# Kernel tuning notes

Measured on AMD Instinct MI355X. Metric: run time of the kernel, lower is better.

The kernel has to match this reference:

```python
import jax, jax.numpy as jnp
import numpy as np

RATIOS = [0.9, 0.7, 0.5, 0.3]
EPS = 1e-5


def _layernorm(x, g, b):
    m = jnp.mean(x, axis=-1, keepdims=True)
    v = jnp.mean(jnp.square(x - m), axis=-1, keepdims=True)
    return (x - m) * jax.lax.rsqrt(v + EPS) * g + b


def _stage(x, g, b, W, bias):
    return _layernorm(x, g, b) @ W + bias


def _prune(x, W1, b1, W2, b2, ratio):
    B, N, C = x.shape
    stats = jnp.mean(x, axis=1)                       # (B, C)
    scores = jax.nn.relu(stats @ W1 + b1) @ W2 + b2    # (B, C)
    k = max(1, int(C * ratio))
    _, idx = jax.lax.top_k(jax.lax.stop_gradient(scores), k)  # (B, k)
    hard = jnp.zeros((B, C), scores.dtype).at[jnp.arange(B)[:, None], idx].set(1.0)
    soft = jax.nn.sigmoid(scores)
    # straight-through: forward value == hard, gradient flows through soft
    mask = hard + soft - jax.lax.stop_gradient(soft)
    return x * mask[:, None, :]


def setup_inputs() -> dict:
    key = jax.random.key(0)
    dims = [(96, 96), (96, 192), (192, 384), (384, 768)]
    inp = {}
    ks = jax.random.split(key, 64)
    ki = iter(ks)
    inp["x"] = jax.random.normal(next(ki), (32, 3136, 96), dtype=jnp.float32)
    for i, (din, dout) in enumerate(dims, 1):
        inp[f"s{i}_g"] = jnp.ones((din,), jnp.float32)
        inp[f"s{i}_b"] = jnp.zeros((din,), jnp.float32)
        inp[f"s{i}_W"] = jax.random.normal(next(ki), (din, dout), jnp.float32) * 0.02
        inp[f"s{i}_bias"] = jnp.zeros((dout,), jnp.float32)
        d = dout
        inp[f"p{i}_W1"] = jax.random.normal(next(ki), (d, d // 4), jnp.float32) * 0.02
        inp[f"p{i}_b1"] = jnp.zeros((d // 4,), jnp.float32)
        inp[f"p{i}_W2"] = jax.random.normal(next(ki), (d // 4, d), jnp.float32) * 0.02
        inp[f"p{i}_b2"] = jnp.zeros((d,), jnp.float32)
    inp["H"] = 56
    inp["W"] = 56
    return inp


def reference(x,
              s1_g, s1_b, s1_W, s1_bias, p1_W1, p1_b1, p1_W2, p1_b2,
              s2_g, s2_b, s2_W, s2_bias, p2_W1, p2_b1, p2_W2, p2_b2,
              s3_g, s3_b, s3_W, s3_bias, p3_W1, p3_b1, p3_W2, p3_b2,
              s4_g, s4_b, s4_W, s4_bias, p4_W1, p4_b1, p4_W2, p4_b2,
              H, W):
    x = _stage(x, s1_g, s1_b, s1_W, s1_bias)
    x = _prune(x, p1_W1, p1_b1, p1_W2, p1_b2, RATIOS[0])
    x = _stage(x, s2_g, s2_b, s2_W, s2_bias)
    x = _prune(x, p2_W1, p2_b1, p2_W2, p2_b2, RATIOS[1])
    x = _stage(x, s3_g, s3_b, s3_W, s3_bias)
    x = _prune(x, p3_W1, p3_b1, p3_W2, p3_b2, RATIOS[2])
    x = _stage(x, s4_g, s4_b, s4_W, s4_bias)
    x = _prune(x, p4_W1, p4_b1, p4_W2, p4_b2, RATIOS[3])
    return x
```

## Files before the change

### kernel.cpp

```cpp
#include <hip/hip_runtime.h>
#include <hip/hip_bf16.h>
#include <stdint.h>

#define NTOK 3136
#define MTOT 100352
#define RPW  14
#define WPB  224

typedef __attribute__((ext_vector_type(8))) short bf16x8;
typedef __attribute__((ext_vector_type(4))) float f32x4;
typedef __attribute__((ext_vector_type(2))) float f32x2;

static __device__ __forceinline__ ushort f2bf(float x) {
  union { float f; uint32_t u; } c; c.f = x;
  uint32_t r = (c.u + 0x7FFFu + ((c.u >> 16) & 1u)) >> 16;
  return (ushort)r;
}
static __device__ __forceinline__ float bf2f(ushort h) {
  union { uint32_t u; float f; } c; c.u = ((uint32_t)h) << 16;
  return c.f;
}

template<int DIN, bool WLO>
__global__ __launch_bounds__(256)
void ln_colsum_k(const float* __restrict__ in, const float* __restrict__ gma,
                 const float* __restrict__ bta, ushort* __restrict__ oh,
                 ushort* __restrict__ ol, float* __restrict__ part)
{
  constexpr int P2 = DIN / 2;
  constexpr int T2 = (P2 + 63) / 64;
  const int wid  = (blockIdx.x * 256 + threadIdx.x) >> 6;
  const int lane = threadIdx.x & 63;
  const int b = wid / WPB;
  const int w = wid - b * WPB;

  f32x2 gv[T2], bv[T2], acc[T2];
#pragma unroll
  for (int t = 0; t < T2; ++t) {
    int c2 = lane + 64 * t;
    if (c2 < P2) {
      gv[t] = *(const f32x2*)(gma + 2 * c2);
      bv[t] = *(const f32x2*)(bta + 2 * c2);
    } else { gv[t] = {0.f, 0.f}; bv[t] = {0.f, 0.f}; }
    acc[t] = {0.f, 0.f};
  }

  const size_t rbase = ((size_t)b * NTOK + (size_t)w * RPW) * DIN;
  const float* ip = in + rbase;
  ushort* oph = oh + rbase;
  ushort* opl = ol + rbase;

  for (int j = 0; j < RPW; ++j) {
    f32x2 v[T2];
    float s = 0.f, sq = 0.f;
#pragma unroll
    for (int t = 0; t < T2; ++t) {
      int c2 = lane + 64 * t;
      f32x2 xv = {0.f, 0.f};
      if (c2 < P2) xv = *(const f32x2*)(ip + (size_t)j * DIN + 2 * c2);
      v[t] = xv;
      s  += xv[0] + xv[1];
      sq += xv[0] * xv[0] + xv[1] * xv[1];
    }
#pragma unroll
    for (int off = 1; off < 64; off <<= 1) {
      s  += __shfl_xor(s, off);
      sq += __shfl_xor(sq, off);
    }
    float m   = s / (float)DIN;
    float var = sq / (float)DIN - m * m;
    float r   = 1.f / sqrtf(var + 1e-5f);
#pragma unroll
    for (int t = 0; t < T2; ++t) {
      int c2 = lane + 64 * t;
      if (c2 < P2) {
        float xn0 = (v[t][0] - m) * r * gv[t][0] + bv[t][0];
        float xn1 = (v[t][1] - m) * r * gv[t][1] + bv[t][1];
        ushort h0 = f2bf(xn0), h1 = f2bf(xn1);
        ((uint32_t*)(oph + (size_t)j * DIN))[c2] =
            (uint32_t)h0 | ((uint32_t)h1 << 16);
        if (WLO) {
          ushort l0 = f2bf(xn0 - bf2f(h0)), l1 = f2bf(xn1 - bf2f(h1));
          ((uint32_t*)(opl + (size_t)j * DIN))[c2] =
              (uint32_t)l0 | ((uint32_t)l1 << 16);
        }
        acc[t][0] += xn0;
        acc[t][1] += xn1;
      }
    }
  }
#pragma unroll
  for (int t = 0; t < T2; ++t) {
    int c2 = lane + 64 * t;
    if (c2 < P2) {
      int c = 2 * c2;
      part[((size_t)b * DIN + c) * WPB + w]     = acc[t][0];
      part[((size_t)b * DIN + c + 1) * WPB + w] = acc[t][1];
    }
  }
}

template<int DIN, int DOUT, int SLOTS, bool CMP, int CMPN>
__global__ __launch_bounds__(1024)
void scores_k(const float* __restrict__ part,
              const float* __restrict__ Wt, const float* __restrict__ bias,
              const float* __restrict__ W1, const float* __restrict__ b1,
              const float* __restrict__ W2, const float* __restrict__ b2,
              float* __restrict__ mask, int k,
              int* __restrict__ list_g, float* __restrict__ biasc)
{
  constexpr int DH  = DOUT / 4;
  constexpr int DH4 = DH / 4;
  constexpr int NSLC = (1024 / DH4 < 64) ? 1024 / DH4 : 64;
  constexpr int RPSC = (DOUT + NSLC - 1) / NSLC;
  constexpr int C4  = DOUT / 4;
  constexpr int NSLD = (1024 / C4 < 64) ? 1024 / C4 : 64;
  constexpr int RPSD = (DH + NSLD - 1) / NSLD;

  __shared__ float xm[DIN];
  __shared__ float st[DOUT];
  __shared__ float h[DH];
  __shared__ float sc[DOUT];
  __shared__ float red[4096];
  __shared__ int lsh[256];

  const int b = blockIdx.x, tid = threadIdx.x;

  if constexpr (SLOTS == 25) {
    if (tid < DIN) {
      const float* p = part + ((size_t)b * DIN + tid) * 25;
      float s = 0.f;
#pragma unroll
      for (int i = 0; i < 25; ++i) s += p[i];
      xm[tid] = s * (1.f / (float)NTOK);
    }
  } else {
    const int cg = tid >> 2, wq = tid & 3;
    if (cg < DIN) {
      const float* p = part + ((size_t)b * DIN + cg) * WPB + wq * 56;
      f32x4 a = {0.f, 0.f, 0.f, 0.f};
#pragma unroll
      for (int u = 0; u < 14; ++u) {
        f32x4 t0 = *(const f32x4*)(p + u * 4);
        a[0] += t0[0]; a[1] += t0[1]; a[2] += t0[2]; a[3] += t0[3];
      }
      red[wq * DIN + cg] = (a[0] + a[1]) + (a[2] + a[3]);
    }
    __syncthreads();
    if (tid < DIN)
      xm[tid] = ((red[0 * DIN + tid] + red[1 * DIN + tid]) +
                 (red[2 * DIN + tid] + red[3 * DIN + tid])) * (1.f / (float)NTOK);
  }
  __syncthreads();

  {
    constexpr int RPS = DIN / 4;
    const int j4 = tid % C4, sl = tid / C4;
    if (sl < 4) {
      const float* wp = Wt + (size_t)(sl * RPS) * DOUT + j4 * 4;
      f32x4 acc = {0.f, 0.f, 0.f, 0.f};
#pragma unroll
      for (int r = 0; r < RPS; ++r) {
        f32x4 wv = *(const f32x4*)(wp + (size_t)r * DOUT);
        float xv = xm[sl * RPS + r];
        acc[0] = fmaf(xv, wv[0], acc[0]);
        acc[1] = fmaf(xv, wv[1], acc[1]);
        acc[2] = fmaf(xv, wv[2], acc[2]);
        acc[3] = fmaf(xv, wv[3], acc[3]);
      }
      *(f32x4*)&red[sl * DOUT + j4 * 4] = acc;
    }
  }
  __syncthreads();
  if (tid < DOUT)
    st[tid] = ((red[0 * DOUT + tid] + red[1 * DOUT + tid]) +
               (red[2 * DOUT + tid] + red[3 * DOUT + tid])) + bias[tid];
  __syncthreads();

  {
    const int j4 = tid % DH4, sl = tid / DH4;
    if (sl < NSLC) {
      f32x4 acc = {0.f, 0.f, 0.f, 0.f};
#pragma unroll
      for (int rr = 0; rr < RPSC; ++rr) {
        int r = sl * RPSC + rr;
        if (r < DOUT) {
          f32x4 wv = *(const f32x4*)(W1 + (size_t)r * DH + j4 * 4);
          float sv = st[r];
          acc[0] = fmaf(sv, wv[0], acc[0]);
          acc[1] = fmaf(sv, wv[1], acc[1]);
          acc[2] = fmaf(sv, wv[2], acc[2]);
          acc[3] = fmaf(sv, wv[3], acc[3]);
        }
      }
      *(f32x4*)&red[(size_t)sl * DH + j4 * 4] = acc;
    }
  }
  __syncthreads();
  if (tid < DH) {
    float a = 0.f;
#pragma unroll 4
    for (int sl = 0; sl < NSLC; ++sl) a += red[(size_t)sl * DH + tid];
    h[tid] = fmaxf(b1[tid] + a, 0.f);
  }
  __syncthreads();

  {
    const int c4 = tid % C4, sl = tid / C4;
    if (sl < NSLD) {
      f32x4 acc = {0.f, 0.f, 0.f, 0.f};
#pragma unroll
      for (int rr = 0; rr < RPSD; ++rr) {
        int r = sl * RPSD + rr;
        if (r < DH) {
          f32x4 wv = *(const f32x4*)(W2 + (size_t)r * DOUT + c4 * 4);
          float hv = h[r];
          acc[0] = fmaf(hv, wv[0], acc[0]);
          acc[1] = fmaf(hv, wv[1], acc[1]);
          acc[2] = fmaf(hv, wv[2], acc[2]);
          acc[3] = fmaf(hv, wv[3], acc[3]);
        }
      }
      *(f32x4*)&red[(size_t)sl * DOUT + c4 * 4] = acc;
    }
  }
  __syncthreads();
  for (int c = tid; c < DOUT; c += 1024) {
    float a = 0.f;
#pragma unroll 4
    for (int sl = 0; sl < NSLD; ++sl) a += red[(size_t)sl * DOUT + c];
    sc[c] = b2[c] + a;
  }
  __syncthreads();

  for (int c = tid; c < DOUT; c += 1024) {
    float v = sc[c];
    int rank = 0;
#pragma unroll 8
    for (int j = 0; j < DOUT; ++j) {
      float u = sc[j];
      rank += (u > v) || (u == v && j < c);
    }
    mask[(size_t)b * DOUT + c] = (rank < k) ? 1.f : 0.f;
    if (CMP && rank < k) lsh[rank] = c;
  }
  if constexpr (CMP) {
    if (tid >= k && tid < CMPN) lsh[tid] = -1;
    __syncthreads();
    if (tid < CMPN) {
      int c = lsh[tid];
      list_g[b * 256 + tid] = c;
      biasc[b * 256 + tid] = (c >= 0) ? bias[c] : 0.f;
    }
  }
}

__global__ __launch_bounds__(256)
void convW_all_k(const float* __restrict__ W0, const float* __restrict__ W1,
                 const float* __restrict__ W2, const float* __restrict__ W3,
                 ushort* __restrict__ hi, ushort* __restrict__ lo)
{
  const int Kd[4]   = { 96, 96, 192, 384 };
  const int Nd[4]   = { 96, 192, 384, 768 };
  const int off[5]  = { 0, 12288, 36864, 110592, 405504 };
  const float* Wp[4] = { W0, W1, W2, W3 };

  int idx = blockIdx.x * 256 + threadIdx.x;
  if (idx >= 405504) return;
  int s = (idx >= off[1]) + (idx >= off[2]) + (idx >= off[3]);
  int local = idx - off[s];
  int K = Kd[s], N = Nd[s];
  int n = local / K, kk = local - n * K;
  float v = (n < N) ? Wp[s][(size_t)kk * N + n] : 0.f;
  ushort h = f2bf(v);
  hi[idx] = h;
  lo[idx] = f2bf(v - bf2f(h));
}

#define ASYNC16(GP, LP) __builtin_amdgcn_global_load_lds( \
    (const __attribute__((address_space(1))) void*)(GP),  \
    (__attribute__((address_space(3))) void*)(LP), 16, 0, 0)

template<int K, int BNL, int N, int NWN, bool WLO>
__global__ __launch_bounds__(128 * NWN)
void gemm_ln_k(const ushort* __restrict__ ahi, const ushort* __restrict__ alo,
               const ushort* __restrict__ bhi, const ushort* __restrict__ blo,
               const float* __restrict__ bias, const float* __restrict__ msk,
               const float* __restrict__ gnext, const float* __restrict__ bnext,
               ushort* __restrict__ oh, ushort* __restrict__ ol,
               float* __restrict__ part)
{
  constexpr int T   = 128 * NWN;
  constexpr int R   = T / 4;
  constexpr int AI  = 128 / R;
  constexpr int BI  = BNL / R;
  constexpr int KS  = K / 32;
  constexpr int WN  = N / NWN;
  constexpr int NFR = WN / 16;
  __shared__ __align__(16) ushort ldsAh[128 * 32];
  __shared__ __align__(16) ushort ldsAl[128 * 32];
  __shared__ __align__(16) ushort ldsBh[BNL * 32];
  __shared__ __align__(16) ushort ldsBl[BNL * 32];

  const int tid  = threadIdx.x;
  const int lane = tid & 63;
  const int wid  = tid >> 6;
  const int wm = wid & 1, wn = wid >> 1;

  const int q8  = gridDim.x >> 3;
  const int bid = blockIdx.x;
  const int mt  = (bid & 7) * q8 + (bid >> 3);
  const size_t row0 = (size_t)mt * 128;

  f32x4 acc[4][NFR];
#pragma unroll
  for (int i = 0; i < 4; ++i)
#pragma unroll
    for (int j = 0; j < NFR; ++j) acc[i][j] = { 0.f, 0.f, 0.f, 0.f };

  const int c_row  = tid >> 2;
  const int c_phys = tid & 3;

#define STG(KK)                                                                \
  {                                                                            \
    const int k0_ = (KK) * 32;                                                 \
    _Pragma("unroll")                                                          \
    for (int r_ = 0; r_ < AI; ++r_) {                                          \
      int row_  = c_row + r_ * R;                                              \
      int slot_ = c_phys ^ ((row_ >> 1) & 3);                                  \
      ASYNC16(ahi + (row0 + row_) * (size_t)K + (k0_ + slot_ * 8),             \
              &ldsAh[(row_ * 4 + c_phys) * 8]);                                \
      ASYNC16(alo + (row0 + row_) * (size_t)K + (k0_ + slot_ * 8),             \
              &ldsAl[(row_ * 4 + c_phys) * 8]);                                \
    }                                                                          \
    _Pragma("unroll")                                                          \
    for (int r_ = 0; r_ < BI; ++r_) {                                          \
      int row_  = c_row + r_ * R;                                              \
      int slot_ = c_phys ^ ((row_ >> 1) & 3);                                  \
      ASYNC16(bhi + (size_t)row_ * K + (k0_ + slot_ * 8),                      \
              &ldsBh[(row_ * 4 + c_phys) * 8]);                                \
      ASYNC16(blo + (size_t)row_ * K + (k0_ + slot_ * 8),                      \
              &ldsBl[(row_ * 4 + c_phys) * 8]);                                \
    }                                                                          \
  }

#pragma unroll
  for (int t = 0; t < KS; ++t) {
    STG(t);
    asm volatile("s_waitcnt vmcnt(0)" ::: "memory");
    __builtin_amdgcn_s_barrier();
    const int slot = lane >> 4;
    const int r16  = lane & 15;
    bf16x8 ah[4], al[4], bh[NFR], bl[NFR];
#pragma unroll
    for (int mi = 0; mi < 4; ++mi) {
      int r = wm * 64 + mi * 16 + r16;
      int off = (r * 4 + (slot ^ ((r >> 1) & 3))) * 8;
      ah[mi] = *(const bf16x8*)&ldsAh[off];
      al[mi] = *(const bf16x8*)&ldsAl[off];
    }
#pragma unroll
    for (int ni = 0; ni < NFR; ++ni) {
      int r = wn * WN + ni * 16 + r16;
      int off = (r * 4 + (slot ^ ((r >> 1) & 3))) * 8;
      bh[ni] = *(const bf16x8*)&ldsBh[off];
      bl[ni] = *(const bf16x8*)&ldsBl[off];
    }
#pragma unroll
    for (int mi = 0; mi < 4; ++mi)
#pragma unroll
      for (int ni = 0; ni < NFR; ++ni)
        acc[mi][ni] = __builtin_amdgcn_mfma_f32_16x16x32_bf16(ah[mi], bh[ni],
                                                              acc[mi][ni], 0, 0, 0);
#pragma unroll
    for (int mi = 0; mi < 4; ++mi)
#pragma unroll
      for (int ni = 0; ni < NFR; ++ni)
        acc[mi][ni] = __builtin_amdgcn_mfma_f32_16x16x32_bf16(ah[mi], bl[ni],
                                                              acc[mi][ni], 0, 0, 0);
#pragma unroll
    for (int mi = 0; mi < 4; ++mi)
#pragma unroll
      for (int ni = 0; ni < NFR; ++ni)
        acc[mi][ni] = __builtin_amdgcn_mfma_f32_16x16x32_bf16(al[mi], bh[ni],
                                                              acc[mi][ni], 0, 0, 0);
    if (t + 1 < KS) __builtin_amdgcn_s_barrier();
  }
#undef STG

  __syncthreads();

  float* rowred = (float*)&ldsAh[0];
  float* colred = (float*)&ldsAl[0];
  ushort* xsh = (ushort*)&ldsBh[0];
  ushort* xsl = (ushort*)&ldsBl[0];

  const int l15 = lane & 15, l4 = lane >> 4;
  const int b0i = (int)(row0 / NTOK);
  const size_t rowB = (size_t)(b0i + 1) * NTOK;
  const bool strad = rowB < row0 + 128;

  float biasv[NFR], mk0a[NFR], mk1a[NFR], gvn[NFR], bvn[NFR];
#pragma unroll
  for (int ni = 0; ni < NFR; ++ni) {
    int n = wn * WN + ni * 16 + l15;
    biasv[ni] = bias[n];
    mk0a[ni] = msk[(size_t)b0i * N + n];
    mk1a[ni] = strad ? msk[(size_t)(b0i + 1) * N + n] : mk0a[ni];
    gvn[ni] = gnext[n];
    bvn[ni] = bnext[n];
  }

  float rs[16], rq[16];
#pragma unroll
  for (int i = 0; i < 16; ++i) { rs[i] = 0.f; rq[i] = 0.f; }
#pragma unroll
  for (int mi = 0; mi < 4; ++mi)
#pragma unroll
    for (int q = 0; q < 4; ++q) {
      size_t row = row0 + wm * 64 + mi * 16 + l4 * 4 + q;
      bool loB = row < rowB;
#pragma unroll
      for (int ni = 0; ni < NFR; ++ni) {
        float v = (acc[mi][ni][q] + biasv[ni]) * (loB ? mk0a[ni] : mk1a[ni]);
        acc[mi][ni][q] = v;
        rs[mi * 4 + q] += v;
        rq[mi * 4 + q] += v * v;
      }
    }
#pragma unroll
  for (int off = 1; off < 16; off <<= 1)
#pragma unroll
    for (int i = 0; i < 16; ++i) {
      rs[i] += __shfl_xor(rs[i], off);
      rq[i] += __shfl_xor(rq[i], off);
    }
  if (l15 == 0) {
#pragma unroll
    for (int mi = 0; mi < 4; ++mi)
#pragma unroll
      for (int q = 0; q < 4; ++q) {
        int r = wm * 64 + mi * 16 + l4 * 4 + q;
        rowred[(wn * 128 + r) * 2 + 0] = rs[mi * 4 + q];
        rowred[(wn * 128 + r) * 2 + 1] = rq[mi * 4 + q];
      }
  }
  __syncthreads();

  float mean[16], rstd[16];
#pragma unroll
  for (int mi = 0; mi < 4; ++mi)
#pragma unroll
    for (int q = 0; q < 4; ++q) {
      int r = wm * 64 + mi * 16 + l4 * 4 + q;
      float S = 0.f, Q = 0.f;
#pragma unroll
      for (int w = 0; w < NWN; ++w) {
        S += rowred[(w * 128 + r) * 2 + 0];
        Q += rowred[(w * 128 + r) * 2 + 1];
      }
      float mn  = S / (float)N;
      float var = Q / (float)N - mn * mn;
      mean[mi * 4 + q] = mn;
      rstd[mi * 4 + q] = 1.f / sqrtf(var + 1e-5f);
    }

  float cs0[NFR], cs1[NFR];
#pragma unroll
  for (int ni = 0; ni < NFR; ++ni) { cs0[ni] = 0.f; cs1[ni] = 0.f; }
#pragma unroll
  for (int mi = 0; mi < 4; ++mi) {
    __syncthreads();
#pragma unroll
    for (int q = 0; q < 4; ++q) {
      const int rl = l4 * 4 + q;
      const size_t row = row0 + wm * 64 + mi * 16 + rl;
      const bool loB = row < rowB;
      const float mn = mean[mi * 4 + q], rv = rstd[mi * 4 + q];
#pragma unroll
      for (int ni = 0; ni < NFR; ++ni) {
        const int n = wn * WN + ni * 16 + l15;
        float xn = (acc[mi][ni][q] - mn) * rv * gvn[ni] + bvn[ni];
        ushort hh = f2bf(xn);
        xsh[(wm * 16 + rl) * N + n] = hh;
        if constexpr (WLO) xsl[(wm * 16 + rl) * N + n] = f2bf(xn - bf2f(hh));
        if (loB) cs0[ni] += xn; else cs1[ni] += xn;
      }
    }
    __syncthreads();
    constexpr int U4R = N / 8;
    for (int idx = tid; idx < 32 * U4R; idx += T) {
      const int grp = idx / U4R, c = idx - grp * U4R;
      const size_t row = row0 + (grp >> 4) * 64 + mi * 16 + (grp & 15);
      *(uint4*)(oh + row * (size_t)N + c * 8) =
          *(const uint4*)(xsh + grp * N + c * 8);
      if constexpr (WLO)
        *(uint4*)(ol + row * (size_t)N + c * 8) =
            *(const uint4*)(xsl + grp * N + c * 8);
    }
  }

#pragma unroll
  for (int ni = 0; ni < NFR; ++ni) {
    cs0[ni] += __shfl_xor(cs0[ni], 16);
    cs0[ni] += __shfl_xor(cs0[ni], 32);
    cs1[ni] += __shfl_xor(cs1[ni], 16);
    cs1[ni] += __shfl_xor(cs1[ni], 32);
  }
  __syncthreads();
  if (l4 == 0) {
#pragma unroll
    for (int ni = 0; ni < NFR; ++ni) {
      int n = wn * WN + ni * 16 + l15;
      colred[(0 * 2 + wm) * N + n] = cs0[ni];
      colred[(1 * 2 + wm) * N + n] = cs1[ni];
    }
  }
  __syncthreads();
  if (wm == 0 && l4 == 0) {
    const int mt_lo = (b0i * NTOK) >> 7;
    const int slot0 = mt - mt_lo;
#pragma unroll
    for (int ni = 0; ni < NFR; ++ni) {
      int n = wn * WN + ni * 16 + l15;
      float t0 = colred[0 * N + n] + colred[1 * N + n];
      part[((size_t)b0i * N + n) * 25 + slot0] = t0;
      if (strad) {
        float t1 = colred[2 * N + n] + colred[3 * N + n];
        part[((size_t)(b0i + 1) * N + n) * 25 + 0] = t1;
      }
    }
  }
}

template<int K, int NC, int N>
__global__ __launch_bounds__(256)
void gemm_lnc_k(const ushort* __restrict__ ahi, const ushort* __restrict__ alo,
                const ushort* __restrict__ whi, const ushort* __restrict__ wlo,
                const int* __restrict__ list, const float* __restrict__ biasc,
                const float* __restrict__ gnext, const float* __restrict__ bnext,
                ushort* __restrict__ oh, float* __restrict__ part)
{
  constexpr int KS  = K / 32;
  constexpr int WN  = NC / 2;
  constexpr int NFR = WN / 16;
  __shared__ __align__(16) ushort ldsAh[2][128 * 32];
  __shared__ __align__(16) ushort ldsAl[2][128 * 32];
  __shared__ __align__(16) ushort ldsBh[2][NC * 32];
  __shared__ __align__(16) ushort ldsBl[2][NC * 32];

  const int tid  = threadIdx.x;
  const int lane = tid & 63;
  const int wid  = tid >> 6;
  const int wm = wid & 1, wn = wid >> 1;

  const int q8  = gridDim.x >> 3;
  const int bid = blockIdx.x;
  const int wg  = (bid & 7) * q8 + (bid >> 3);
  const int b   = wg / 25;
  const int mt  = wg - b * 25;
  const size_t row0 = (size_t)b * NTOK + (size_t)mt * 128;
  const size_t rowEnd = (size_t)(b + 1) * NTOK;
  const int rows_valid = (mt == 24) ? 64 : 128;

  const int c_row  = tid >> 2;
  const int c_phys = tid & 3;

  int bsrc[3];
#pragma unroll
  for (int r_ = 0; r_ < 3; ++r_) {
    int s = list[b * 256 + c_row + r_ * 64];
    bsrc[r_] = (s < 0) ? 0 : s;
  }

  f32x4 acc[4][NFR];
#pragma unroll
  for (int i = 0; i < 4; ++i)
#pragma unroll
    for (int j = 0; j < NFR; ++j) acc[i][j] = { 0.f, 0.f, 0.f, 0.f };

#define STGL(BUF, KK)                                                          \
  {                                                                            \
    const int k0_ = (KK) * 32;                                                 \
    _Pragma("unroll")                                                          \
    for (int r_ = 0; r_ < 2; ++r_) {                                           \
      int row_  = c_row + r_ * 64;                                             \
      int slot_ = c_phys ^ ((row_ >> 1) & 3);                                  \
      size_t ar_ = row0 + row_;                                                \
      if (ar_ >= rowEnd) ar_ = rowEnd - 1;                                     \
      ASYNC16(ahi + ar_ * (size_t)K + (k0_ + slot_ * 8),                       \
              &ldsAh[BUF][(row_ * 4 + c_phys) * 8]);                           \
      ASYNC16(alo + ar_ * (size_t)K + (k0_ + slot_ * 8),                       \
              &ldsAl[BUF][(row_ * 4 + c_phys) * 8]);                           \
    }                                                                          \
    _Pragma("unroll")                                                          \
    for (int r_ = 0; r_ < 3; ++r_) {                                           \
      int row_  = c_row + r_ * 64;                                             \
      int slot_ = c_phys ^ ((row_ >> 1) & 3);                                  \
      ASYNC16(whi + (size_t)bsrc[r_] * K + (k0_ + slot_ * 8),                  \
              &ldsBh[BUF][(row_ * 4 + c_phys) * 8]);                           \
      ASYNC16(wlo + (size_t)bsrc[r_] * K + (k0_ + slot_ * 8),                  \
              &ldsBl[BUF][(row_ * 4 + c_phys) * 8]);                           \
    }                                                                          \
  }

  STGL(0, 0);
  asm volatile("s_waitcnt vmcnt(0)" ::: "memory");
  __builtin_amdgcn_s_barrier();
#pragma unroll
  for (int t = 0; t < KS; ++t) {
    if (t + 1 < KS) STGL((t + 1) & 1, t + 1);
    const int buf = t & 1;
    const int slot = lane >> 4;
    const int r16  = lane & 15;
    bf16x8 ah[4], al[4], bh[NFR], bl[NFR];
#pragma unroll
    for (int mi = 0; mi < 4; ++mi) {
      int r = wm * 64 + mi * 16 + r16;
      int off = (r * 4 + (slot ^ ((r >> 1) & 3))) * 8;
      ah[mi] = *(const bf16x8*)&ldsAh[buf][off];
      al[mi] = *(const bf16x8*)&ldsAl[buf][off];
    }
#pragma unroll
    for (int ni = 0; ni < NFR; ++ni) {
      int r = wn * WN + ni * 16 + r16;
      int off = (r * 4 + (slot ^ ((r >> 1) & 3))) * 8;
      bh[ni] = *(const bf16x8*)&ldsBh[buf][off];
      bl[ni] = *(const bf16x8*)&ldsBl[buf][off];
    }
#pragma unroll
    for (int mi = 0; mi < 4; ++mi)
#pragma unroll
      for (int ni = 0; ni < NFR; ++ni)
        acc[mi][ni] = __builtin_amdgcn_mfma_f32_16x16x32_bf16(ah[mi], bh[ni],
                                                              acc[mi][ni], 0, 0, 0);
#pragma unroll
    for (int mi = 0; mi < 4; ++mi)
#pragma unroll
      for (int ni = 0; ni < NFR; ++ni)
        acc[mi][ni] = __builtin_amdgcn_mfma_f32_16x16x32_bf16(ah[mi], bl[ni],
                                                              acc[mi][ni], 0, 0, 0);
#pragma unroll
    for (int mi = 0; mi < 4; ++mi)
#pragma unroll
      for (int ni = 0; ni < NFR; ++ni)
        acc[mi][ni] = __builtin_amdgcn_mfma_f32_16x16x32_bf16(al[mi], bh[ni],
                                                              acc[mi][ni], 0, 0, 0);
    if (t + 1 < KS) {
      asm volatile("s_waitcnt vmcnt(0)" ::: "memory");
      __builtin_amdgcn_s_barrier();
    }
  }
#undef STGL

  __syncthreads();

  float* rr      = (float*)&ldsAh[0][0];
  float* rowredp = rr;
  float* rowmnrv = rr + 512;
  float* rowrv   = rr + 640;
  float* sbuf    = (float*)&ldsBh[0][0];

  const int l15 = lane & 15, l4 = lane >> 4;

  int   nj[NFR];
  float biasv[NFR];
#pragma unroll
  for (int ni = 0; ni < NFR; ++ni) {
    int j = wn * WN + ni * 16 + l15;
    nj[ni]    = list[b * 256 + j];
    biasv[ni] = biasc[b * 256 + j];
  }

  float rs[16], rq[16];
#pragma unroll
  for (int i = 0; i < 16; ++i) { rs[i] = 0.f; rq[i] = 0.f; }
#pragma unroll
  for (int mi = 0; mi < 4; ++mi)
#pragma unroll
    for (int q = 0; q < 4; ++q) {
#pragma unroll
      for (int ni = 0; ni < NFR; ++ni) {
        float v = acc[mi][ni][q] + biasv[ni];
        acc[mi][ni][q] = v;
        rs[mi * 4 + q] += v;
        rq[mi * 4 + q] += v * v;
      }
    }
#pragma unroll
  for (int off = 1; off < 16; off <<= 1)
#pragma unroll
    for (int i = 0; i < 16; ++i) {
      rs[i] += __shfl_xor(rs[i], off);
      rq[i] += __shfl_xor(rq[i], off);
    }
  if (l15 == 0) {
#pragma unroll
    for (int mi = 0; mi < 4; ++mi)
#pragma unroll
      for (int q = 0; q < 4; ++q) {
        int r = wm * 64 + mi * 16 + l4 * 4 + q;
        rowredp[(wn * 128 + r) * 2 + 0] = rs[mi * 4 + q];
        rowredp[(wn * 128 + r) * 2 + 1] = rq[mi * 4 + q];
      }
  }
  __syncthreads();
  if (tid < 128) {
    float S = rowredp[(0 * 128 + tid) * 2 + 0] + rowredp[(1 * 128 + tid) * 2 + 0];
    float Q = rowredp[(0 * 128 + tid) * 2 + 1] + rowredp[(1 * 128 + tid) * 2 + 1];
    float mn = S / (float)N;
    float rv = 1.f / sqrtf(Q / (float)N - mn * mn + 1e-5f);
    rowmnrv[tid] = mn * rv;
    rowrv[tid]   = rv;
  }
  __syncthreads();

  float colS = 0.f, colS2 = 0.f;

#pragma unroll
  for (int h = 0; h < 8; ++h) {
    if (h * 16 >= rows_valid) break;
    __syncthreads();
    for (int idx = tid; idx < 16 * N / 4; idx += 256)
      ((f32x4*)sbuf)[idx] = f32x4{0.f, 0.f, 0.f, 0.f};
    __syncthreads();
    if ((h >> 2) == wm) {
      const int mi = h & 3;
#pragma unroll
      for (int q = 0; q < 4; ++q) {
        const int rl = l4 * 4 + q;
        const float rv = rowrv[h * 16 + rl];
#pragma unroll
        for (int ni = 0; ni < NFR; ++ni)
          sbuf[rl * N + nj[ni]] = acc[mi][ni][q] * rv;
      }
    }
    __syncthreads();
    {
      float a = 0.f;
#pragma unroll
      for (int rl = 0; rl < 16; ++rl) a += sbuf[rl * N + tid];
      colS += a;
      if (tid < N - 256) {
        float a2 = 0.f;
        const int c2 = 256 + tid;
#pragma unroll
        for (int rl = 0; rl < 16; ++rl) a2 += sbuf[rl * N + c2];
        colS2 += a2;
      }
    }
    for (int idx = tid; idx < 16 * (N / 8); idx += 256) {
      const int rl = idx / (N / 8), cg = idx - rl * (N / 8);
      const float mnrv = rowmnrv[h * 16 + rl];
      const float* sp = sbuf + rl * N + cg * 8;
      f32x4 s0 = *(const f32x4*)(sp);
      f32x4 s1 = *(const f32x4*)(sp + 4);
      f32x4 g0 = *(const f32x4*)(gnext + cg * 8);
      f32x4 g1 = *(const f32x4*)(gnext + cg * 8 + 4);
      f32x4 e0 = *(const f32x4*)(bnext + cg * 8);
      f32x4 e1 = *(const f32x4*)(bnext + cg * 8 + 4);
      uint32_t w[4];
#pragma unroll
      for (int j = 0; j < 2; ++j) {
        ushort ha = f2bf(g0[2*j]   * (s0[2*j]   - mnrv) + e0[2*j]);
        ushort hb = f2bf(g0[2*j+1] * (s0[2*j+1] - mnrv) + e0[2*j+1]);
        w[j] = (uint32_t)ha | ((uint32_t)hb << 16);
      }
#pragma unroll
      for (int j = 0; j < 2; ++j) {
        ushort ha = f2bf(g1[2*j]   * (s1[2*j]   - mnrv) + e1[2*j]);
        ushort hb = f2bf(g1[2*j+1] * (s1[2*j+1] - mnrv) + e1[2*j+1]);
        w[2 + j] = (uint32_t)ha | ((uint32_t)hb << 16);
      }
      *(uint4*)(oh + (row0 + h * 16 + rl) * (size_t)N + cg * 8) =
          make_uint4(w[0], w[1], w[2], w[3]);
    }
  }

  float msum = 0.f;
  for (int r = 0; r < rows_valid; ++r) msum += rowmnrv[r];
  {
    const int c = tid;
    part[((size_t)b * N + c) * 25 + mt] =
        gnext[c] * (colS - msum) + (float)rows_valid * bnext[c];
    if (tid < N - 256) {
      const int c2 = 256 + tid;
      part[((size_t)b * N + c2) * 25 + mt] =
          gnext[c2] * (colS2 - msum) + (float)rows_valid * bnext[c2];
    }
  }
}

template<int K>
__global__ __launch_bounds__(512)
void gemm_c4_k(const ushort* __restrict__ A, const ushort* __restrict__ whi,
               const int* __restrict__ list, const float* __restrict__ biasc,
               float* __restrict__ C)
{
  constexpr int NT = K / 32;
  __shared__ __align__(16) ushort ldsA[3][128 * 32];
  __shared__ __align__(16) ushort ldsB[3][256 * 32];

  const int tid  = threadIdx.x;
  const int lane = tid & 63;
  const int wid  = tid >> 6;
  const int wm = wid & 1, wn = wid >> 1;

  const int q8  = gridDim.x >> 3;
  const int bid = blockIdx.x;
  const int wg  = (bid & 7) * q8 + (bid >> 3);
  const int b   = wg / 25;
  const int mt  = wg - b * 25;
  const size_t row0 = (size_t)b * NTOK + (size_t)mt * 128;
  const int rows_valid = (mt == 24) ? 64 : 128;

  const int c_row  = tid >> 2;
  const int c_phys = tid & 3;

  size_t arow = row0 + c_row;
  const size_t rowEnd = (size_t)(b + 1) * NTOK;
  if (arow >= rowEnd) arow = rowEnd - 1;
  const ushort* apr = A + arow * (size_t)K;

  int bsrc[2];
#pragma unroll
  for (int r_ = 0; r_ < 2; ++r_) {
    int s = list[b * 256 + c_row + r_ * 128];
    bsrc[r_] = (s < 0) ? 0 : s;
  }

  f32x4 acc[4][4];
#pragma unroll
  for (int i = 0; i < 4; ++i)
#pragma unroll
    for (int j = 0; j < 4; ++j) acc[i][j] = { 0.f, 0.f, 0.f, 0.f };

#define STAGEC(BUF, TT)                                                        \
  {                                                                            \
    const int k0_ = (TT) * 32;                                                 \
    {                                                                          \
      int slot_ = c_phys ^ ((c_row >> 1) & 3);                                 \
      ASYNC16(apr + (k0_ + slot_ * 8),                                         \
              &ldsA[BUF][(c_row * 4 + c_phys) * 8]);                           \
    }                                                                          \
    _Pragma("unroll")                                                          \
    for (int r_ = 0; r_ < 2; ++r_) {                                           \
      int row_  = c_row + r_ * 128;                                            \
      int slot_ = c_phys ^ ((row_ >> 1) & 3);                                  \
      ASYNC16(whi + (size_t)bsrc[r_] * K + (k0_ + slot_ * 8),                  \
              &ldsB[BUF][(row_ * 4 + c_phys) * 8]);                            \
    }                                                                          \
  }

  STAGEC(0, 0);
  STAGEC(1, 1);
#pragma unroll
  for (int t = 0; t < NT; ++t) {
    if (t == NT - 1) { asm volatile("s_waitcnt vmcnt(0)" ::: "memory"); }
    else             { asm volatile("s_waitcnt vmcnt(3)" ::: "memory"); }
    __builtin_amdgcn_s_barrier();
    if (t + 2 < NT) STAGEC((t + 2) % 3, t + 2);
    const int buf = t % 3;
    const int slot = lane >> 4;
    const int r16  = lane & 15;
    bf16x8 af[4], bfr[4];
#pragma unroll
    for (int mi = 0; mi < 4; ++mi) {
      int r = wm * 64 + mi * 16 + r16;
      af[mi] = *(const bf16x8*)&ldsA[buf][(r * 4 + (slot ^ ((r >> 1) & 3))) * 8];
    }
#pragma unroll
    for (int ni = 0; ni < 4; ++ni) {
      int r = wn * 64 + ni * 16 + r16;
      bfr[ni] = *(const bf16x8*)&ldsB[buf][(r * 4 + (slot ^ ((r >> 1) & 3))) * 8];
    }
#pragma unroll
    for (int mi = 0; mi < 4; ++mi)
#pragma unroll
      for (int ni = 0; ni < 4; ++ni)
        acc[mi][ni] = __builtin_amdgcn_mfma_f32_16x16x32_bf16(af[mi], bfr[ni],
                                                              acc[mi][ni], 0, 0, 0);
  }
#undef STAGEC

  float* cst = (float*)&ldsB[0][0];

  const int l15 = lane & 15, l4 = lane >> 4;
  int   nj[4];
  float biasv[4];
#pragma unroll
  for (int ni = 0; ni < 4; ++ni) {
    int j = wn * 64 + ni * 16 + l15;
    nj[ni]    = list[b * 256 + j];
    biasv[ni] = biasc[b * 256 + j];
  }

#pragma unroll
  for (int hh = 0; hh < 8; ++hh) {
    const int hrows = rows_valid - hh * 16;
    if (hrows <= 0) break;
    __syncthreads();
    for (int idx = tid; idx < 16 * 192; idx += 512)
      ((f32x4*)cst)[idx] = f32x4{0.f, 0.f, 0.f, 0.f};
    __syncthreads();
    if ((hh >> 2) == wm) {
      const int mi = hh & 3;
#pragma unroll
      for (int q = 0; q < 4; ++q) {
        const int rl = l4 * 4 + q;
#pragma unroll
        for (int ni = 0; ni < 4; ++ni)
          if (nj[ni] >= 0)
            cst[rl * 768 + nj[ni]] = acc[mi][ni][q] + biasv[ni];
      }
    }
    __syncthreads();
    const int nst = (hrows >= 16 ? 16 : hrows) * 192;
    for (int idx = tid; idx < nst; idx += 512) {
      const int grp = idx / 192, c = idx - grp * 192;
      const size_t row = row0 + hh * 16 + grp;
      *(f32x4*)(C + row * 768 + c * 4) = ((const f32x4*)cst)[grp * 192 + c];
    }
  }
}

extern "C" void kernel_launch(void* const* d_in, const int* in_sizes, int n_in,
                              void* d_out, int out_size, void* d_ws, size_t ws_size,
                              hipStream_t stream)
{
  (void)in_sizes; (void)n_in; (void)out_size; (void)ws_size;
  const float* x = (const float*)d_in[0];
  const float *sg[4], *sb[4], *sW[4], *sbias[4], *pW1[4], *pb1[4], *pW2[4], *pb2[4];
  for (int s = 0; s < 4; ++s) {
    int base = 1 + s * 8;
    sg[s]    = (const float*)d_in[base + 0];
    sb[s]    = (const float*)d_in[base + 1];
    sW[s]    = (const float*)d_in[base + 2];
    sbias[s] = (const float*)d_in[base + 3];
    pW1[s]   = (const float*)d_in[base + 4];
    pb1[s]   = (const float*)d_in[base + 5];
    pW2[s]   = (const float*)d_in[base + 6];
    pb2[s]   = (const float*)d_in[base + 7];
  }

  float* out = (float*)d_out;
  ushort* hiA = (ushort*)out;
  ushort* loA = (ushort*)(out + 19267584);
  ushort* loB = (ushort*)(out + 38535168);

  char* ws = (char*)d_ws;
  ushort* hiB  = (ushort*)(ws);
  float*  part = (float*) (ws + 77070336);
  float*  mk   = (float*) (ws + 79822848);
  ushort* w_hi = (ushort*)(ws + 79921152);
  ushort* w_lo = (ushort*)(ws + 80732160);
  int*    lst  = (int*)   (ws + 87834624);
  float*  bsc  = (float*) (ws + 87867392);

  const int woff[4] = { 0, 12288, 36864, 110592 };

  convW_all_k<<<(405504 + 255) / 256, 256, 0, stream>>>(
      sW[0], sW[1], sW[2], sW[3], w_hi, w_lo);

  const int LNG = 32 * WPB / 4;

  ln_colsum_k<96, true><<<LNG, 256, 0, stream>>>(x, sg[0], sb[0], hiA, loA, part);
  scores_k<96, 96, 224, false, 256><<<32, 1024, 0, stream>>>(
      part, sW[0], sbias[0], pW1[0], pb1[0], pW2[0], pb2[0], mk, 86,
      nullptr, nullptr);
  gemm_ln_k<96, 128, 96, 2, true><<<784, 256, 0, stream>>>(
      hiA, loA, w_hi + woff[0], w_lo + woff[0],
      sbias[0], mk, sg[1], sb[1], hiB, loB, part);

  scores_k<96, 192, 25, false, 256><<<32, 1024, 0, stream>>>(
      part, sW[1], sbias[1], pW1[1], pb1[1], pW2[1], pb2[1], mk, 134,
      nullptr, nullptr);
  gemm_ln_k<96, 192, 192, 2, true><<<784, 256, 0, stream>>>(
      hiB, loB, w_hi + woff[1], w_lo + woff[1],
      sbias[1], mk, sg[2], sb[2], hiA, loA, part);

  scores_k<192, 384, 25, true, 192><<<32, 1024, 0, stream>>>(
      part, sW[2], sbias[2], pW1[2], pb1[2], pW2[2], pb2[2], mk, 192,
      lst, bsc);
  gemm_lnc_k<192, 192, 384><<<800, 256, 0, stream>>>(
      hiA, loA, w_hi + woff[2], w_lo + woff[2], lst, bsc, sg[3], sb[3],
      hiB, part);

  scores_k<384, 768, 25, true, 256><<<32, 1024, 0, stream>>>(
      part, sW[3], sbias[3], pW1[3], pb1[3], pW2[3], pb2[3], mk, 230,
      lst, bsc);
  gemm_c4_k<384><<<800, 512, 0, stream>>>(hiB, w_hi + woff[3], lst, bsc, out);
}
```

Baseline: 452.9 us.

## Rewrite first LayerNorm as block-tiled kernel and single-buffer gemm_lnc LDS

The first-stage LayerNorm kernel now gives each row to four threads with vectorized loads and stores. Column sums are reduced in shared memory per 64-row tile, which cuts the partial-sum slots from 224 to 49 and simplifies the reduction in scores_k. In gemm_lnc_k the double-buffered LDS staging is replaced by a single buffer that loads and then waits each K step. This halves shared memory to allow more resident blocks, but it gives up overlap between global loads and MFMA compute.

```diff
diff --git a/kernel.cpp b/kernel.cpp
--- a/kernel.cpp
+++ b/kernel.cpp
@@ -4,8 +4,6 @@
 
 #define NTOK 3136
 #define MTOT 100352
-#define RPW  14
-#define WPB  224
 
 typedef __attribute__((ext_vector_type(8))) short bf16x8;
 typedef __attribute__((ext_vector_type(4))) float f32x4;
@@ -21,82 +19,68 @@
   return c.f;
 }
 
-template<int DIN, bool WLO>
 __global__ __launch_bounds__(256)
-void ln_colsum_k(const float* __restrict__ in, const float* __restrict__ gma,
-                 const float* __restrict__ bta, ushort* __restrict__ oh,
-                 ushort* __restrict__ ol, float* __restrict__ part)
+void ln1_k(const float* __restrict__ in, const float* __restrict__ gma,
+           const float* __restrict__ bta, ushort* __restrict__ oh,
+           ushort* __restrict__ ol, float* __restrict__ part)
 {
-  constexpr int P2 = DIN / 2;
-  constexpr int T2 = (P2 + 63) / 64;
-  const int wid  = (blockIdx.x * 256 + threadIdx.x) >> 6;
-  const int lane = threadIdx.x & 63;
-  const int b = wid / WPB;
-  const int w = wid - b * WPB;
-
-  f32x2 gv[T2], bv[T2], acc[T2];
-#pragma unroll
-  for (int t = 0; t < T2; ++t) {
-    int c2 = lane + 64 * t;
-    if (c2 < P2) {
-      gv[t] = *(const f32x2*)(gma + 2 * c2);
-      bv[t] = *(const f32x2*)(bta + 2 * c2);
-    } else { gv[t] = {0.f, 0.f}; bv[t] = {0.f, 0.f}; }
-    acc[t] = {0.f, 0.f};
-  }
-
-  const size_t rbase = ((size_t)b * NTOK + (size_t)w * RPW) * DIN;
-  const float* ip = in + rbase;
-  ushort* oph = oh + rbase;
-  ushort* opl = ol + rbase;
-
-  for (int j = 0; j < RPW; ++j) {
-    f32x2 v[T2];
-    float s = 0.f, sq = 0.f;
-#pragma unroll
-    for (int t = 0; t < T2; ++t) {
-      int c2 = lane + 64 * t;
-      f32x2 xv = {0.f, 0.f};
-      if (c2 < P2) xv = *(const f32x2*)(ip + (size_t)j * DIN + 2 * c2);
-      v[t] = xv;
-      s  += xv[0] + xv[1];
-      sq += xv[0] * xv[0] + xv[1] * xv[1];
-    }
-#pragma unroll
-    for (int off = 1; off < 64; off <<= 1) {
-      s  += __shfl_xor(s, off);
-      sq += __shfl_xor(sq, off);
-    }
-    float m   = s / (float)DIN;
-    float var = sq / (float)DIN - m * m;
-    float r   = 1.f / sqrtf(var + 1e-5f);
-#pragma unroll
-    for (int t = 0; t < T2; ++t) {
-      int c2 = lane + 64 * t;
-      if (c2 < P2) {
-        float xn0 = (v[t][0] - m) * r * gv[t][0] + bv[t][0];
-        float xn1 = (v[t][1] - m) * r * gv[t][1] + bv[t][1];
-        ushort h0 = f2bf(xn0), h1 = f2bf(xn1);
-        ((uint32_t*)(oph + (size_t)j * DIN))[c2] =
-            (uint32_t)h0 | ((uint32_t)h1 << 16);
-        if (WLO) {
-          ushort l0 = f2bf(xn0 - bf2f(h0)), l1 = f2bf(xn1 - bf2f(h1));
-          ((uint32_t*)(opl + (size_t)j * DIN))[c2] =
-              (uint32_t)l0 | ((uint32_t)l1 << 16);
-        }
-        acc[t][0] += xn0;
-        acc[t][1] += xn1;
-      }
-    }
-  }
-#pragma unroll
-  for (int t = 0; t < T2; ++t) {
-    int c2 = lane + 64 * t;
-    if (c2 < P2) {
-      int c = 2 * c2;
-      part[((size_t)b * DIN + c) * WPB + w]     = acc[t][0];
-      part[((size_t)b * DIN + c + 1) * WPB + w] = acc[t][1];
-    }
+  __shared__ float red[64][104];
+  const int tid = threadIdx.x;
+  const int g = tid >> 2, sub = tid & 3;
+  const int blk = blockIdx.x;
+  const int b = blk / 49, t49 = blk - b * 49;
+  const size_t row = (size_t)b * NTOK + (size_t)t49 * 64 + g;
+  const float* ip = in + row * 96 + sub * 24;
+
+  f32x4 v[6];
+  float s = 0.f, sq = 0.f;
+#pragma unroll
+  for (int u = 0; u < 6; ++u) {
+    v[u] = *(const f32x4*)(ip + u * 4);
+    s  += (v[u][0] + v[u][1]) + (v[u][2] + v[u][3]);
+    sq += (v[u][0]*v[u][0] + v[u][1]*v[u][1]) +
+          (v[u][2]*v[u][2] + v[u][3]*v[u][3]);
+  }
+  s  += __shfl_xor(s, 1);  s  += __shfl_xor(s, 2);
+  sq += __shfl_xor(sq, 1); sq += __shfl_xor(sq, 2);
+  const float m   = s * (1.f / 96.f);
+  const float var = sq * (1.f / 96.f) - m * m;
+  const float r   = 1.f / sqrtf(var + 1e-5f);
+
+  uint32_t hiw[12], low[12];
+#pragma unroll
+  for (int u = 0; u < 6; ++u) {
+    f32x4 gv = *(const f32x4*)(gma + sub * 24 + u * 4);
+    f32x4 bv = *(const f32x4*)(bta + sub * 24 + u * 4);
+    f32x4 xn;
+#pragma unroll
+    for (int e = 0; e < 4; ++e) xn[e] = (v[u][e] - m) * r * gv[e] + bv[e];
+    *(f32x4*)&red[g][sub * 24 + u * 4] = xn;
+    ushort h0 = f2bf(xn[0]), h1 = f2bf(xn[1]);
+    ushort h2 = f2bf(xn[2]), h3 = f2bf(xn[3]);
+    hiw[2*u]   = (uint32_t)h0 | ((uint32_t)h1 << 16);
+    hiw[2*u+1] = (uint32_t)h2 | ((uint32_t)h3 << 16);
+    ushort l0 = f2bf(xn[0] - bf2f(h0)), l1 = f2bf(xn[1] - bf2f(h1));
+    ushort l2 = f2bf(xn[2] - bf2f(h2)), l3 = f2bf(xn[3] - bf2f(h3));
+    low[2*u]   = (uint32_t)l0 | ((uint32_t)l1 << 16);
+    low[2*u+1] = (uint32_t)l2 | ((uint32_t)l3 << 16);
+  }
+  {
+    ushort* op = oh + row * 96 + sub * 24;
+    *(uint4*)(op + 0)  = make_uint4(hiw[0], hiw[1], hiw[2],  hiw[3]);
+    *(uint4*)(op + 8)  = make_uint4(hiw[4], hiw[5], hiw[6],  hiw[7]);
+    *(uint4*)(op + 16) = make_uint4(hiw[8], hiw[9], hiw[10], hiw[11]);
+    ushort* opl = ol + row * 96 + sub * 24;
+    *(uint4*)(opl + 0)  = make_uint4(low[0], low[1], low[2],  low[3]);
+    *(uint4*)(opl + 8)  = make_uint4(low[4], low[5], low[6],  low[7]);
+    *(uint4*)(opl + 16) = make_uint4(low[8], low[9], low[10], low[11]);
+  }
+  __syncthreads();
+  if (tid < 96) {
+    float a = 0.f;
+#pragma unroll 8
+    for (int g2 = 0; g2 < 64; ++g2) a += red[g2][tid];
+    part[((size_t)b * 96 + tid) * 49 + t49] = a;
   }
 }
 
@@ -126,30 +110,12 @@
 
   const int b = blockIdx.x, tid = threadIdx.x;
 
-  if constexpr (SLOTS == 25) {
-    if (tid < DIN) {
-      const float* p = part + ((size_t)b * DIN + tid) * 25;
-      float s = 0.f;
-#pragma unroll
-      for (int i = 0; i < 25; ++i) s += p[i];
-      xm[tid] = s * (1.f / (float)NTOK);
-    }
-  } else {
-    const int cg = tid >> 2, wq = tid & 3;
-    if (cg < DIN) {
-      const float* p = part + ((size_t)b * DIN + cg) * WPB + wq * 56;
-      f32x4 a = {0.f, 0.f, 0.f, 0.f};
-#pragma unroll
-      for (int u = 0; u < 14; ++u) {
-        f32x4 t0 = *(const f32x4*)(p + u * 4);
-        a[0] += t0[0]; a[1] += t0[1]; a[2] += t0[2]; a[3] += t0[3];
-      }
-      red[wq * DIN + cg] = (a[0] + a[1]) + (a[2] + a[3]);
-    }
-    __syncthreads();
-    if (tid < DIN)
-      xm[tid] = ((red[0 * DIN + tid] + red[1 * DIN + tid]) +
-                 (red[2 * DIN + tid] + red[3 * DIN + tid])) * (1.f / (float)NTOK);
+  if (tid < DIN) {
+    const float* p = part + ((size_t)b * DIN + tid) * SLOTS;
+    float s = 0.f;
+#pragma unroll
+    for (int i = 0; i < SLOTS; ++i) s += p[i];
+    xm[tid] = s * (1.f / (float)NTOK);
   }
   __syncthreads();
 
@@ -544,10 +510,11 @@
   constexpr int KS  = K / 32;
   constexpr int WN  = NC / 2;
   constexpr int NFR = WN / 16;
-  __shared__ __align__(16) ushort ldsAh[2][128 * 32];
-  __shared__ __align__(16) ushort ldsAl[2][128 * 32];
-  __shared__ __align__(16) ushort ldsBh[2][NC * 32];
-  __shared__ __align__(16) ushort ldsBl[2][NC * 32];
+  __shared__ __align__(16) ushort lds[2 * 128 * 32 + 2 * NC * 32];
+  ushort* ldsAh = lds;
+  ushort* ldsAl = lds + 128 * 32;
+  ushort* ldsBh = lds + 2 * 128 * 32;
+  ushort* ldsBl = lds + 2 * 128 * 32 + NC * 32;
 
   const int tid  = threadIdx.x;
   const int lane = tid & 63;
@@ -579,7 +546,7 @@
 #pragma unroll
     for (int j = 0; j < NFR; ++j) acc[i][j] = { 0.f, 0.f, 0.f, 0.f };
 
-#define STGL(BUF, KK)                                                          \
+#define STGL(KK)                                                               \
   {                                                                            \
     const int k0_ = (KK) * 32;                                                 \
     _Pragma("unroll")                                                          \
@@ -589,28 +556,26 @@
       size_t ar_ = row0 + row_;                                                \
       if (ar_ >= rowEnd) ar_ = rowEnd - 1;                                     \
       ASYNC16(ahi + ar_ * (size_t)K + (k0_ + slot_ * 8),                       \
-              &ldsAh[BUF][(row_ * 4 + c_phys) * 8]);                           \
+              &ldsAh[(row_ * 4 + c_phys) * 8]);                                \
       ASYNC16(alo + ar_ * (size_t)K + (k0_ + slot_ * 8),                       \
-              &ldsAl[BUF][(row_ * 4 + c_phys) * 8]);                           \
+              &ldsAl[(row_ * 4 + c_phys) * 8]);                                \
     }                                                                          \
     _Pragma("unroll")                                                          \
     for (int r_ = 0; r_ < 3; ++r_) {                                           \
       int row_  = c_row + r_ * 64;                                             \
       int slot_ = c_phys ^ ((row_ >> 1) & 3);                                  \
       ASYNC16(whi + (size_t)bsrc[r_] * K + (k0_ + slot_ * 8),                  \
-              &ldsBh[BUF][(row_ * 4 + c_phys) * 8]);                           \
+              &ldsBh[(row_ * 4 + c_phys) * 8]);                                \
       ASYNC16(wlo + (size_t)bsrc[r_] * K + (k0_ + slot_ * 8),                  \
-              &ldsBl[BUF][(row_ * 4 + c_phys) * 8]);                           \
+              &ldsBl[(row_ * 4 + c_phys) * 8]);                                \
     }                                                                          \
   }
 
-  STGL(0, 0);
-  asm volatile("s_waitcnt vmcnt(0)" ::: "memory");
-  __builtin_amdgcn_s_barrier();
 #pragma unroll
   for (int t = 0; t < KS; ++t) {
-    if (t + 1 < KS) STGL((t + 1) & 1, t + 1);
-    const int buf = t & 1;
+    STGL(t);
+    asm volatile("s_waitcnt vmcnt(0)" ::: "memory");
+    __builtin_amdgcn_s_barrier();
     const int slot = lane >> 4;
     const int r16  = lane & 15;
     bf16x8 ah[4], al[4], bh[NFR], bl[NFR];
@@ -618,15 +583,15 @@
     for (int mi = 0; mi < 4; ++mi) {
       int r = wm * 64 + mi * 16 + r16;
       int off = (r * 4 + (slot ^ ((r >> 1) & 3))) * 8;
-      ah[mi] = *(const bf16x8*)&ldsAh[buf][off];
-      al[mi] = *(const bf16x8*)&ldsAl[buf][off];
+      ah[mi] = *(const bf16x8*)&ldsAh[off];
+      al[mi] = *(const bf16x8*)&ldsAl[off];
     }
 #pragma unroll
     for (int ni = 0; ni < NFR; ++ni) {
       int r = wn * WN + ni * 16 + r16;
       int off = (r * 4 + (slot ^ ((r >> 1) & 3))) * 8;
-      bh[ni] = *(const bf16x8*)&ldsBh[buf][off];
-      bl[ni] = *(const bf16x8*)&ldsBl[buf][off];
+      bh[ni] = *(const bf16x8*)&ldsBh[off];
+      bl[ni] = *(const bf16x8*)&ldsBl[off];
     }
 #pragma unroll
     for (int mi = 0; mi < 4; ++mi)
@@ -646,20 +611,17 @@
       for (int ni = 0; ni < NFR; ++ni)
         acc[mi][ni] = __builtin_amdgcn_mfma_f32_16x16x32_bf16(al[mi], bh[ni],
                                                               acc[mi][ni], 0, 0, 0);
-    if (t + 1 < KS) {
-      asm volatile("s_waitcnt vmcnt(0)" ::: "memory");
-      __builtin_amdgcn_s_barrier();
-    }
+    if (t + 1 < KS) __builtin_amdgcn_s_barrier();
   }
 #undef STGL
 
   __syncthreads();
 
-  float* rr      = (float*)&ldsAh[0][0];
+  float* rr      = (float*)ldsAh;
   float* rowredp = rr;
   float* rowmnrv = rr + 512;
   float* rowrv   = rr + 640;
-  float* sbuf    = (float*)&ldsBh[0][0];
+  float* sbuf    = (float*)ldsBh;
 
   const int l15 = lane & 15, l4 = lane >> 4;
 
@@ -962,10 +924,8 @@
   convW_all_k<<<(405504 + 255) / 256, 256, 0, stream>>>(
       sW[0], sW[1], sW[2], sW[3], w_hi, w_lo);
 
-  const int LNG = 32 * WPB / 4;
-
-  ln_colsum_k<96, true><<<LNG, 256, 0, stream>>>(x, sg[0], sb[0], hiA, loA, part);
-  scores_k<96, 96, 224, false, 256><<<32, 1024, 0, stream>>>(
+  ln1_k<<<32 * 49, 256, 0, stream>>>(x, sg[0], sb[0], hiA, loA, part);
+  scores_k<96, 96, 49, false, 256><<<32, 1024, 0, stream>>>(
       part, sW[0], sbias[0], pW1[0], pb1[0], pW2[0], pb2[0], mk, 86,
       nullptr, nullptr);
   gemm_ln_k<96, 128, 96, 2, true><<<784, 256, 0, stream>>>(
```

After: 443.2 us. -2.1%, faster.
